# Optimization experiments

Measured on AMD Instinct MI355X. Metric: run time of the kernel, lower is better.

## Reference

```python
import jax, jax.numpy as jnp
import numpy as np

ALPHA = 1.0
GAMMA = 0.8
TAU = 0.1
NUM_SAMPLES = 10
TOP_K = 100
NUM_USER_GROUPS = 8
NUM_ITEM_GROUPS = 16
BATCH = 1024
NUM_ITEMS = 10000


def setup_inputs() -> dict:
    key = jax.random.key(0)
    k1, k2, k3, k4 = jax.random.split(key, 4)
    pred_scores = jax.random.normal(k1, (BATCH, NUM_ITEMS), dtype=jnp.float32)
    true_scores = jax.random.uniform(k2, (BATCH, NUM_ITEMS), dtype=jnp.float32)
    user_groups = jax.random.randint(k3, (BATCH,), 0, NUM_USER_GROUPS)
    item_groups = jax.random.randint(k4, (NUM_ITEMS,), 0, NUM_ITEM_GROUPS)
    return {
        "pred_scores": pred_scores,
        "true_scores": true_scores,
        "user_groups": user_groups,
        "item_groups": item_groups,
    }


def _calculate_exposure(scores):
    # scores: [B, k]. Soft-rank via Gumbel perturbations + pairwise sigmoid.
    B, k = scores.shape
    noise = jax.random.gumbel(jax.random.key(1), (NUM_SAMPLES, B, k), dtype=scores.dtype)
    noisy = scores[None, :, :] + noise                       # [S, B, k]
    diffs = noisy[..., :, None] - noisy[..., None, :]        # [S, B, k, k]
    # ranks = 1 + sum_j sigmoid((s_i - s_j)/tau) - sigmoid(0)
    ranks = 1.0 + jax.nn.sigmoid(diffs / TAU).sum(axis=-1) - 0.5  # [S, B, k]
    exposure = jnp.power(GAMMA, ranks - 1.0)                 # [S, B, k]
    return exposure.mean(axis=0)                             # [B, k]


def reference(pred_scores, true_scores, user_groups, item_groups):
    B = pred_scores.shape[0]
    # top-k selection (values == gathered pred scores)
    pred_topk, topk_idx = jax.lax.top_k(pred_scores, TOP_K)   # [B, k]
    item_groups_topk = item_groups[topk_idx]                  # [B, k]

    system_exposure = _calculate_exposure(pred_topk)          # [B, k]
    target_exposure = jnp.full_like(system_exposure, true_scores.mean())
    delta_E = system_exposure - target_exposure               # [B, k]

    ii_f_loss = jnp.mean(delta_E * delta_E)

    # group-pair scatter_mean
    pair_ids = user_groups[:, None] * NUM_ITEM_GROUPS + item_groups_topk  # [B, k]
    flat = delta_E.reshape(-1)
    pid = pair_ids.reshape(-1)
    num_pairs = NUM_USER_GROUPS * NUM_ITEM_GROUPS
    sums = jax.ops.segment_sum(flat, pid, num_segments=num_pairs)
    cnts = jax.ops.segment_sum(jnp.ones_like(flat), pid, num_segments=num_pairs)
    avg = jnp.where(cnts > 0, sums / jnp.maximum(cnts, 1.0), 0.0)
    gg_f_loss = jnp.mean(avg * avg)

    total_loss = ii_f_loss + ALPHA * gg_f_loss
    return (total_loss, ii_f_loss, gg_f_loss)
```

## Files before the change

kernel.cpp:

```cpp
#include <hip/hip_runtime.h>


typedef unsigned int u32;
typedef unsigned long long u64;

__device__ __forceinline__ u32 rotl32(u32 x, int r) { return (x << r) | (x >> (32 - r)); }

__device__ __forceinline__ void tf2x32(u32 k0, u32 k1, u32 x0, u32 x1, u32& o0, u32& o1) {
  u32 ks2 = 0x1BD11BDAu ^ k0 ^ k1;
#define TFR(r) { x0 += x1; x1 = rotl32(x1, r); x1 ^= x0; }
  x0 += k0; x1 += k1;
  TFR(13) TFR(15) TFR(26) TFR(6)
  x0 += k1; x1 += ks2 + 1u;
  TFR(17) TFR(29) TFR(16) TFR(24)
  x0 += ks2; x1 += k0 + 2u;
  TFR(13) TFR(15) TFR(26) TFR(6)
  x0 += k0; x1 += k1 + 3u;
  TFR(17) TFR(29) TFR(16) TFR(24)
  x0 += k1; x1 += ks2 + 4u;
  TFR(13) TFR(15) TFR(26) TFR(6)
  x0 += ks2; x1 += k0 + 5u;
#undef TFR
  o0 = x0; o1 = x1;
}

__device__ __forceinline__ float gumbel_noise(u32 i) {
  u32 o0, o1;
  tf2x32(0u, 1u, 0u, i, o0, o1);
  u32 bits = o0 ^ o1;
  float f = __uint_as_float((bits >> 9) | 0x3f800000u) - 1.0f;
  const float TINY = 1.17549435e-38f;
  float u = fmaxf(TINY, f + TINY);
  return -logf(-logf(u));
}

__device__ __forceinline__ u32 fkey(float v) {
  u32 u = __float_as_uint(v);
  return u ^ ((u & 0x80000000u) ? 0xFFFFFFFFu : 0x80000000u);
}

__global__ __launch_bounds__(256) void fused_kernel(
    const float* __restrict__ pred,
    const float* __restrict__ ts,
    const int*   __restrict__ ugrp,
    const int*   __restrict__ igrp,
    double* __restrict__ t_sum,
    double* __restrict__ sum_e, double* __restrict__ sum_e2,
    double* __restrict__ pair_sum, int* __restrict__ pair_cnt) {
  const int N = 10000, N4 = 2500, K = 100;
  const int b = blockIdx.x;
  const int t = threadIdx.x;

  __shared__ u32 hist[256];
  __shared__ u32 ckey[1024];
  __shared__ u64 sbuf[128];
  __shared__ float topv[100];
  __shared__ int   pidv[100];
  __shared__ __align__(16) float noisy[1000];
  __shared__ float expo[100];
  __shared__ float pairS[128];
  __shared__ int   pairC[128];
  __shared__ float wred[4];
  __shared__ u32 sh_cnt, sh_n2, sh_T, sh_A, sh_done;
  __shared__ float sh_bS, sh_bS2;

  hist[t] = 0u;
  if (t < 128) { pairS[t] = 0.f; pairC[t] = 0; }
  if (t < 100) expo[t] = 0.f;
  if (t == 0) { sh_cnt = 0u; sh_n2 = 0u; sh_done = 0u; sh_bS = 0.f; sh_bS2 = 0.f; }
  __syncthreads();

  const float4* row4 = (const float4*)(pred + (size_t)b * N);
  const float4* tsr4 = (const float4*)(ts + (size_t)b * N);

  float tsum = 0.f;
  for (int i4 = t; i4 < N4; i4 += 256) {
    float4 p = row4[i4];
    float4 q = tsr4[i4];
    tsum += (q.x + q.y) + (q.z + q.w);
    atomicAdd(&hist[fkey(p.x) >> 24], 1u);
    atomicAdd(&hist[fkey(p.y) >> 24], 1u);
    atomicAdd(&hist[fkey(p.z) >> 24], 1u);
    atomicAdd(&hist[fkey(p.w) >> 24], 1u);
  }
  for (int off = 32; off; off >>= 1) tsum += __shfl_down(tsum, off);
  if ((t & 63) == 0) wred[t >> 6] = tsum;
  __syncthreads();
  if (t == 0) {
    atomicAdd(t_sum, (double)((wred[0] + wred[1]) + (wred[2] + wred[3])));
    u32 cum = 0, b0 = 255;
    for (int v = 255; v >= 0; --v) {
      u32 c = hist[v];
      if (cum + c >= 100u) { b0 = (u32)v; break; }
      cum += c;
    }
    sh_A = cum;
    sh_T = b0 << 24;
    sh_done = (cum + hist[b0] <= 128u) ? 1u : 0u;
  }
  __syncthreads();

  if (!sh_done) {
    u32 b0 = sh_T >> 24;
    for (int i4 = t; i4 < N4; i4 += 256) {
      float4 p = row4[i4];
#pragma unroll
      for (int c = 0; c < 4; ++c) {
        float v = c == 0 ? p.x : c == 1 ? p.y : c == 2 ? p.z : p.w;
        u32 key = fkey(v);
        if ((key >> 24) == b0) {
          u32 pos = atomicAdd(&sh_cnt, 1u);
          if (pos < 1024u) ckey[pos] = key;
        }
      }
    }
    __syncthreads();
    u32 nk = sh_cnt < 1024u ? sh_cnt : 1024u;
    for (int shift = 16; shift >= 0; shift -= 8) {
      hist[t] = 0u;
      __syncthreads();
      u32 prefhi = sh_T >> (shift + 8);
      for (int i = t; i < (int)nk; i += 256) {
        u32 key = ckey[i];
        if ((key >> (shift + 8)) == prefhi) atomicAdd(&hist[(key >> shift) & 0xFFu], 1u);
      }
      __syncthreads();
      if (t == 0) {
        u32 target = 100u - sh_A;
        u32 cum = 0, bb = 255;
        for (int v = 255; v >= 0; --v) {
          u32 c = hist[v];
          if (cum + c >= target) { bb = (u32)v; break; }
          cum += c;
        }
        sh_A += cum;
        sh_T |= (u32)bb << shift;
        sh_done = (sh_A + hist[bb] <= 128u || shift == 0) ? 1u : 0u;
      }
      __syncthreads();
      if (sh_done) break;
    }
  }

  {
    u32 T = sh_T;
    for (int i4 = t; i4 < N4; i4 += 256) {
      float4 p = row4[i4];
#pragma unroll
      for (int c = 0; c < 4; ++c) {
        int i = i4 * 4 + c;
        float v = c == 0 ? p.x : c == 1 ? p.y : c == 2 ? p.z : p.w;
        u32 key = fkey(v);
        if (key >= T) {
          u32 pos = atomicAdd(&sh_n2, 1u);
          if (pos < 128u) sbuf[pos] = ((u64)key << 32) | (u32)(~(u32)i);
        }
      }
    }
    __syncthreads();
    u32 n2 = sh_n2 < 128u ? sh_n2 : 128u;
    if (t < 128 && (u32)t >= n2) sbuf[t] = 0ull;
    __syncthreads();
  }

  for (int k = 2; k <= 128; k <<= 1) {
    for (int j = k >> 1; j > 0; j >>= 1) {
      if (t < 128) {
        int ixj = t ^ j;
        if (ixj > t) {
          u64 a = sbuf[t], c2 = sbuf[ixj];
          bool up = (t & k) == 0;
          if (up ? (a < c2) : (a > c2)) { sbuf[t] = c2; sbuf[ixj] = a; }
        }
      }
      __syncthreads();
    }
  }

  int ug = ugrp[b];
  if (t < K) {
    u64 p = sbuf[t];
    u32 key = (u32)(p >> 32);
    u32 idx = ~(u32)p;
    u32 u = (key & 0x80000000u) ? (key ^ 0x80000000u) : ~key;
    topv[t] = __uint_as_float(u);
    pidv[t] = ug * 16 + igrp[idx];
  }
  __syncthreads();

  for (int si = t; si < 1000; si += 256) {
    int s = si / 100, i = si - s * 100;
    noisy[si] = topv[i] + gumbel_noise(((u32)s * 1024u + (u32)b) * 100u + (u32)i);
  }
  __syncthreads();

  const float C2 = 14.426950408889634f;
  const float LG = -0.32192809488736235f;
  for (int si = t; si < 1000; si += 256) {
    int s = si / 100, i = si - s * 100;
    float nv = noisy[si];
    float nvC = nv * C2;
    const float* nrow = &noisy[s * 100];
    float S = 0.f;
#pragma unroll 4
    for (int j = 0; j < 100; ++j) {
      float a = __builtin_fmaf(nrow[j], C2, -nvC);
      S += __builtin_amdgcn_rcpf(1.0f + exp2f(a));
    }
    float ex = exp2f((S - 0.5f) * LG);
    atomicAdd(&expo[i], ex);
  }
  __syncthreads();

  if (t < K) {
    float e = expo[t] * 0.1f;
    atomicAdd(&pairS[pidv[t]], e);
    atomicAdd(&pairC[pidv[t]], 1);
    atomicAdd(&sh_bS, e);
    atomicAdd(&sh_bS2, e * e);
  }
  __syncthreads();
  if (t < 128 && pairC[t] > 0) {
    atomicAdd(&pair_sum[t], (double)pairS[t]);
    atomicAdd(&pair_cnt[t], pairC[t]);
  }
  if (t == 0) {
    atomicAdd(sum_e, (double)sh_bS);
    atomicAdd(sum_e2, (double)sh_bS2);
  }
}

__global__ void finalize_kernel(const double* __restrict__ t_sum,
                                const double* __restrict__ sum_e,
                                const double* __restrict__ sum_e2,
                                const double* __restrict__ pair_sum,
                                const int* __restrict__ pair_cnt,
                                float* __restrict__ out) {
  if (threadIdx.x == 0 && blockIdx.x == 0) {
    double t = *t_sum / 10240000.0;
    double me = *sum_e / 102400.0;
    double me2 = *sum_e2 / 102400.0;
    double ii = me2 - 2.0 * t * me + t * t;
    double gg = 0.0;
    for (int p = 0; p < 128; ++p) {
      int c = pair_cnt[p];
      if (c > 0) {
        double avg = (pair_sum[p] - (double)c * t) / (double)c;
        gg += avg * avg;
      }
    }
    gg /= 128.0;
    out[0] = (float)(ii + gg);
    out[1] = (float)ii;
    out[2] = (float)gg;
  }
}

extern "C" void kernel_launch(void* const* d_in, const int* in_sizes, int n_in,
                              void* d_out, int out_size, void* d_ws, size_t ws_size,
                              hipStream_t stream) {
  (void)in_sizes; (void)n_in; (void)out_size; (void)ws_size;
  const float* pred = (const float*)d_in[0];
  const float* ts   = (const float*)d_in[1];
  const int*   ugrp = (const int*)d_in[2];
  const int*   igrp = (const int*)d_in[3];
  float* out = (float*)d_out;

  double* t_sum    = (double*)d_ws;
  double* sum_e    = t_sum + 1;
  double* sum_e2   = t_sum + 2;
  double* pair_sum = t_sum + 3;
  int*    pair_cnt = (int*)(t_sum + 3 + 128);

  hipMemsetAsync(d_ws, 0, (3 + 128) * sizeof(double) + 128 * sizeof(int), stream);

  fused_kernel<<<1024, 256, 0, stream>>>(pred, ts, ugrp, igrp,
                                         t_sum, sum_e, sum_e2, pair_sum, pair_cnt);
  finalize_kernel<<<1, 64, 0, stream>>>(t_sum, sum_e, sum_e2, pair_sum, pair_cnt, out);
}
```

Before: 208.0 us.

## Rework top-k radix select with wave-parallel bin search, candidate cache, rank sort

Raises the block size to 512 threads and splits the first histogram into four privatised copies to reduce LDS atomic contention. The serial single-thread bin scan is replaced by a 64-lane wave suffix-scan. Candidates at or above the first-level bin are cached with their indices, so later refinement and collection passes avoid re-reading global memory, with a global-memory fallback on overflow. The bitonic sort becomes a parallel rank-counting sort, the sigmoid inner loop uses float4 LDS reads, and the finalize kernel uses a parallel reduction. The larger block and extra shared arrays may cut occupancy.

```diff
diff --git a/kernel.cpp b/kernel.cpp
--- a/kernel.cpp
+++ b/kernel.cpp
@@ -39,7 +39,37 @@
   return u ^ ((u & 0x80000000u) ? 0xFFFFFFFFu : 0x80000000u);
 }
 
-__global__ __launch_bounds__(256) void fused_kernel(
+__device__ __forceinline__ void select_bin(const u32* __restrict__ hist, int shift,
+                                           u32* sh_T, u32* sh_A, u32* sh_done,
+                                           int lane) {
+  u32 prevA = *sh_A;
+  u32 target = 100u - prevA;
+  u32 c0 = hist[lane * 4 + 0], c1 = hist[lane * 4 + 1];
+  u32 c2 = hist[lane * 4 + 2], c3 = hist[lane * 4 + 3];
+  u32 s = c0 + c1 + c2 + c3;
+  u32 suf = s;
+#pragma unroll
+  for (int off = 1; off < 64; off <<= 1) {
+    u32 o = __shfl_down(suf, off);
+    suf += (lane + off < 64) ? o : 0u;
+  }
+  u32 sufx = suf - s;
+  if (sufx < target && suf >= target) {
+    u32 cc[4] = {c0, c1, c2, c3};
+    u32 acc = sufx, bin = 0, cnt = 0;
+#pragma unroll
+    for (int k = 3; k >= 0; --k) {
+      if (acc + cc[k] >= target) { bin = (u32)(lane * 4 + k); cnt = cc[k]; break; }
+      acc += cc[k];
+    }
+    u32 newA = prevA + acc;
+    *sh_T = *sh_T | (bin << shift);
+    *sh_A = newA;
+    *sh_done = (newA + cnt <= 128u || shift == 0) ? 1u : 0u;
+  }
+}
+
+__global__ __launch_bounds__(512, 8) void fused_kernel(
     const float* __restrict__ pred,
     const float* __restrict__ ts,
     const int*   __restrict__ ugrp,
@@ -51,92 +81,107 @@
   const int b = blockIdx.x;
   const int t = threadIdx.x;
 
-  __shared__ u32 hist[256];
-  __shared__ u32 ckey[1024];
+  __shared__ u32 hist4[4][256];
+  __shared__ u64 cand[2048];
   __shared__ u64 sbuf[128];
+  __shared__ u64 sorted[128];
+  __shared__ u32 rankv[128];
   __shared__ float topv[100];
   __shared__ int   pidv[100];
   __shared__ __align__(16) float noisy[1000];
   __shared__ float expo[100];
   __shared__ float pairS[128];
   __shared__ int   pairC[128];
-  __shared__ float wred[4];
-  __shared__ u32 sh_cnt, sh_n2, sh_T, sh_A, sh_done;
+  __shared__ float wred[8];
+  __shared__ u32 sh_cnt, sh_nc, sh_T, sh_A, sh_done, sh_ovf;
   __shared__ float sh_bS, sh_bS2;
 
-  hist[t] = 0u;
-  if (t < 128) { pairS[t] = 0.f; pairC[t] = 0; }
+  if (t < 256) { hist4[0][t] = 0u; hist4[1][t] = 0u; hist4[2][t] = 0u; hist4[3][t] = 0u; }
+  if (t < 128) { pairS[t] = 0.f; pairC[t] = 0; rankv[t] = 0u; }
   if (t < 100) expo[t] = 0.f;
-  if (t == 0) { sh_cnt = 0u; sh_n2 = 0u; sh_done = 0u; sh_bS = 0.f; sh_bS2 = 0.f; }
-  __syncthreads();
-
-  const float4* row4 = (const float4*)(pred + (size_t)b * N);
-  const float4* tsr4 = (const float4*)(ts + (size_t)b * N);
+  if (t == 0) { sh_cnt = 0u; sh_nc = 0u; sh_T = 0u; sh_A = 0u; sh_done = 0u; sh_ovf = 0u;
+                sh_bS = 0.f; sh_bS2 = 0.f; }
+  __syncthreads();
+
+  const float4* __restrict__ row4 = (const float4*)(pred + (size_t)b * N);
+  const float4* __restrict__ tsr4 = (const float4*)(ts + (size_t)b * N);
 
   float tsum = 0.f;
-  for (int i4 = t; i4 < N4; i4 += 256) {
-    float4 p = row4[i4];
-    float4 q = tsr4[i4];
-    tsum += (q.x + q.y) + (q.z + q.w);
-    atomicAdd(&hist[fkey(p.x) >> 24], 1u);
-    atomicAdd(&hist[fkey(p.y) >> 24], 1u);
-    atomicAdd(&hist[fkey(p.z) >> 24], 1u);
-    atomicAdd(&hist[fkey(p.w) >> 24], 1u);
-  }
+  u32* myh = hist4[(t >> 7) & 3];
+#pragma unroll
+  for (int k = 0; k < 5; ++k) {
+    int i4 = t + (k << 9);
+    if (k == 4 && i4 >= N4) break;
+    float4 pp = row4[i4];
+    float4 qq = tsr4[i4];
+    tsum += (qq.x + qq.y) + (qq.z + qq.w);
+    atomicAdd(&myh[fkey(pp.x) >> 24], 1u);
+    atomicAdd(&myh[fkey(pp.y) >> 24], 1u);
+    atomicAdd(&myh[fkey(pp.z) >> 24], 1u);
+    atomicAdd(&myh[fkey(pp.w) >> 24], 1u);
+  }
+#pragma unroll
   for (int off = 32; off; off >>= 1) tsum += __shfl_down(tsum, off);
   if ((t & 63) == 0) wred[t >> 6] = tsum;
   __syncthreads();
   if (t == 0) {
-    atomicAdd(t_sum, (double)((wred[0] + wred[1]) + (wred[2] + wred[3])));
-    u32 cum = 0, b0 = 255;
-    for (int v = 255; v >= 0; --v) {
-      u32 c = hist[v];
-      if (cum + c >= 100u) { b0 = (u32)v; break; }
-      cum += c;
-    }
-    sh_A = cum;
-    sh_T = b0 << 24;
-    sh_done = (cum + hist[b0] <= 128u) ? 1u : 0u;
-  }
-  __syncthreads();
-
-  if (!sh_done) {
+    float s8 = 0.f;
+#pragma unroll
+    for (int w = 0; w < 8; ++w) s8 += wred[w];
+    atomicAdd(t_sum, (double)s8);
+  }
+  if (t < 256) hist4[0][t] += hist4[1][t] + hist4[2][t] + hist4[3][t];
+  __syncthreads();
+
+  if (t < 64) select_bin(&hist4[0][0], 24, &sh_T, &sh_A, &sh_done, t);
+  __syncthreads();
+
+  bool r1done = (sh_done != 0u);
+  bool use_cand = false;
+  u32 nc = 0;
+
+  if (!r1done) {
     u32 b0 = sh_T >> 24;
-    for (int i4 = t; i4 < N4; i4 += 256) {
-      float4 p = row4[i4];
+    for (int i4 = t; i4 < N4; i4 += 512) {
+      float4 pp = row4[i4];
 #pragma unroll
       for (int c = 0; c < 4; ++c) {
-        float v = c == 0 ? p.x : c == 1 ? p.y : c == 2 ? p.z : p.w;
+        float v = (c == 0) ? pp.x : (c == 1) ? pp.y : (c == 2) ? pp.z : pp.w;
         u32 key = fkey(v);
-        if ((key >> 24) == b0) {
+        if ((key >> 24) >= b0) {
           u32 pos = atomicAdd(&sh_cnt, 1u);
-          if (pos < 1024u) ckey[pos] = key;
+          int idx = i4 * 4 + c;
+          if (pos < 2048u) cand[pos] = ((u64)key << 32) | (u32)(~(u32)idx);
+          else sh_ovf = 1u;
         }
       }
     }
     __syncthreads();
-    u32 nk = sh_cnt < 1024u ? sh_cnt : 1024u;
-    for (int shift = 16; shift >= 0; shift -= 8) {
-      hist[t] = 0u;
+    nc = sh_cnt < 2048u ? sh_cnt : 2048u;
+    use_cand = (sh_ovf == 0u);
+
+    for (int shift = 16; ; shift -= 8) {
+      if (t < 256) hist4[0][t] = 0u;
       __syncthreads();
-      u32 prefhi = sh_T >> (shift + 8);
-      for (int i = t; i < (int)nk; i += 256) {
-        u32 key = ckey[i];
-        if ((key >> (shift + 8)) == prefhi) atomicAdd(&hist[(key >> shift) & 0xFFu], 1u);
+      u32 pref = sh_T >> (shift + 8);
+      if (use_cand) {
+        for (int i = t; i < (int)nc; i += 512) {
+          u32 key = (u32)(cand[i] >> 32);
+          if ((key >> (shift + 8)) == pref) atomicAdd(&hist4[0][(key >> shift) & 255u], 1u);
+        }
+      } else {
+        for (int i4 = t; i4 < N4; i4 += 512) {
+          float4 pp = row4[i4];
+#pragma unroll
+          for (int c = 0; c < 4; ++c) {
+            float v = (c == 0) ? pp.x : (c == 1) ? pp.y : (c == 2) ? pp.z : pp.w;
+            u32 key = fkey(v);
+            if ((key >> (shift + 8)) == pref) atomicAdd(&hist4[0][(key >> shift) & 255u], 1u);
+          }
+        }
       }
       __syncthreads();
-      if (t == 0) {
-        u32 target = 100u - sh_A;
-        u32 cum = 0, bb = 255;
-        for (int v = 255; v >= 0; --v) {
-          u32 c = hist[v];
-          if (cum + c >= target) { bb = (u32)v; break; }
-          cum += c;
-        }
-        sh_A += cum;
-        sh_T |= (u32)bb << shift;
-        sh_done = (sh_A + hist[bb] <= 128u || shift == 0) ? 1u : 0u;
-      }
+      if (t < 64) select_bin(&hist4[0][0], shift, &sh_T, &sh_A, &sh_done, t);
       __syncthreads();
       if (sh_done) break;
     }
@@ -144,51 +189,60 @@
 
   {
     u32 T = sh_T;
-    for (int i4 = t; i4 < N4; i4 += 256) {
-      float4 p = row4[i4];
-#pragma unroll
-      for (int c = 0; c < 4; ++c) {
-        int i = i4 * 4 + c;
-        float v = c == 0 ? p.x : c == 1 ? p.y : c == 2 ? p.z : p.w;
-        u32 key = fkey(v);
-        if (key >= T) {
-          u32 pos = atomicAdd(&sh_n2, 1u);
-          if (pos < 128u) sbuf[pos] = ((u64)key << 32) | (u32)(~(u32)i);
+    if (use_cand) {
+      for (int i = t; i < (int)nc; i += 512) {
+        u64 p = cand[i];
+        if ((u32)(p >> 32) >= T) {
+          u32 pos = atomicAdd(&sh_nc, 1u);
+          if (pos < 128u) sbuf[pos] = p;
         }
       }
-    }
-    __syncthreads();
-    u32 n2 = sh_n2 < 128u ? sh_n2 : 128u;
-    if (t < 128 && (u32)t >= n2) sbuf[t] = 0ull;
-    __syncthreads();
-  }
-
-  for (int k = 2; k <= 128; k <<= 1) {
-    for (int j = k >> 1; j > 0; j >>= 1) {
-      if (t < 128) {
-        int ixj = t ^ j;
-        if (ixj > t) {
-          u64 a = sbuf[t], c2 = sbuf[ixj];
-          bool up = (t & k) == 0;
-          if (up ? (a < c2) : (a > c2)) { sbuf[t] = c2; sbuf[ixj] = a; }
+    } else {
+      for (int i4 = t; i4 < N4; i4 += 512) {
+        float4 pp = row4[i4];
+#pragma unroll
+        for (int c = 0; c < 4; ++c) {
+          float v = (c == 0) ? pp.x : (c == 1) ? pp.y : (c == 2) ? pp.z : pp.w;
+          u32 key = fkey(v);
+          if (key >= T) {
+            u32 pos = atomicAdd(&sh_nc, 1u);
+            int idx = i4 * 4 + c;
+            if (pos < 128u) sbuf[pos] = ((u64)key << 32) | (u32)(~(u32)idx);
+          }
         }
       }
-      __syncthreads();
-    }
+    }
+    __syncthreads();
+    u32 nreal = sh_nc < 128u ? sh_nc : 128u;
+    if (t < 128 && (u32)t >= nreal) sbuf[t] = 0ull;
+    __syncthreads();
+  }
+
+  {
+    int e = t >> 2, seg = t & 3;
+    u64 mykey = sbuf[e];
+    u32 cnt = 0;
+    int j0 = seg * 32;
+#pragma unroll 8
+    for (int j = j0; j < j0 + 32; ++j) cnt += (sbuf[j] > mykey) ? 1u : 0u;
+    if (cnt) atomicAdd(&rankv[e], cnt);
+    __syncthreads();
+    if (t < 128) sorted[rankv[t]] = sbuf[t];
+    __syncthreads();
   }
 
   int ug = ugrp[b];
   if (t < K) {
-    u64 p = sbuf[t];
-    u32 key = (u32)(p >> 32);
-    u32 idx = ~(u32)p;
+    u64 pk = sorted[t];
+    u32 key = (u32)(pk >> 32);
+    u32 idx = ~(u32)pk;
     u32 u = (key & 0x80000000u) ? (key ^ 0x80000000u) : ~key;
     topv[t] = __uint_as_float(u);
     pidv[t] = ug * 16 + igrp[idx];
   }
   __syncthreads();
 
-  for (int si = t; si < 1000; si += 256) {
+  for (int si = t; si < 1000; si += 512) {
     int s = si / 100, i = si - s * 100;
     noisy[si] = topv[i] + gumbel_noise(((u32)s * 1024u + (u32)b) * 100u + (u32)i);
   }
@@ -196,16 +250,18 @@
 
   const float C2 = 14.426950408889634f;
   const float LG = -0.32192809488736235f;
-  for (int si = t; si < 1000; si += 256) {
+  for (int si = t; si < 1000; si += 512) {
     int s = si / 100, i = si - s * 100;
-    float nv = noisy[si];
-    float nvC = nv * C2;
-    const float* nrow = &noisy[s * 100];
+    float nvC = noisy[si] * C2;
+    const float4* nr4 = (const float4*)(noisy + s * 100);
     float S = 0.f;
-#pragma unroll 4
-    for (int j = 0; j < 100; ++j) {
-      float a = __builtin_fmaf(nrow[j], C2, -nvC);
-      S += __builtin_amdgcn_rcpf(1.0f + exp2f(a));
+#pragma unroll 5
+    for (int jc = 0; jc < 25; ++jc) {
+      float4 nj = nr4[jc];
+      S += __builtin_amdgcn_rcpf(1.0f + exp2f(__builtin_fmaf(nj.x, C2, -nvC)));
+      S += __builtin_amdgcn_rcpf(1.0f + exp2f(__builtin_fmaf(nj.y, C2, -nvC)));
+      S += __builtin_amdgcn_rcpf(1.0f + exp2f(__builtin_fmaf(nj.z, C2, -nvC)));
+      S += __builtin_amdgcn_rcpf(1.0f + exp2f(__builtin_fmaf(nj.w, C2, -nvC)));
     }
     float ex = exp2f((S - 0.5f) * LG);
     atomicAdd(&expo[i], ex);
@@ -230,26 +286,31 @@
   }
 }
 
-__global__ void finalize_kernel(const double* __restrict__ t_sum,
-                                const double* __restrict__ sum_e,
-                                const double* __restrict__ sum_e2,
-                                const double* __restrict__ pair_sum,
-                                const int* __restrict__ pair_cnt,
-                                float* __restrict__ out) {
-  if (threadIdx.x == 0 && blockIdx.x == 0) {
-    double t = *t_sum / 10240000.0;
+__global__ __launch_bounds__(128) void finalize_kernel(
+    const double* __restrict__ t_sum, const double* __restrict__ sum_e,
+    const double* __restrict__ sum_e2, const double* __restrict__ pair_sum,
+    const int* __restrict__ pair_cnt, float* __restrict__ out) {
+  int t = threadIdx.x;
+  __shared__ double red[128];
+  double tmean = *t_sum / 10240000.0;
+  double g = 0.0;
+  int c = pair_cnt[t];
+  if (c > 0) {
+    double avg = (pair_sum[t] - (double)c * tmean) / (double)c;
+    g = avg * avg;
+  }
+  red[t] = g;
+  __syncthreads();
+#pragma unroll
+  for (int off = 64; off; off >>= 1) {
+    if (t < off) red[t] += red[t + off];
+    __syncthreads();
+  }
+  if (t == 0) {
+    double gg = red[0] / 128.0;
     double me = *sum_e / 102400.0;
     double me2 = *sum_e2 / 102400.0;
-    double ii = me2 - 2.0 * t * me + t * t;
-    double gg = 0.0;
-    for (int p = 0; p < 128; ++p) {
-      int c = pair_cnt[p];
-      if (c > 0) {
-        double avg = (pair_sum[p] - (double)c * t) / (double)c;
-        gg += avg * avg;
-      }
-    }
-    gg /= 128.0;
+    double ii = me2 - 2.0 * tmean * me + tmean * tmean;
     out[0] = (float)(ii + gg);
     out[1] = (float)ii;
     out[2] = (float)gg;
@@ -274,7 +335,7 @@
 
   hipMemsetAsync(d_ws, 0, (3 + 128) * sizeof(double) + 128 * sizeof(int), stream);
 
-  fused_kernel<<<1024, 256, 0, stream>>>(pred, ts, ugrp, igrp,
+  fused_kernel<<<1024, 512, 0, stream>>>(pred, ts, ugrp, igrp,
                                          t_sum, sum_e, sum_e2, pair_sum, pair_cnt);
-  finalize_kernel<<<1, 64, 0, stream>>>(t_sum, sum_e, sum_e2, pair_sum, pair_cnt, out);
-}
+  finalize_kernel<<<1, 128, 0, stream>>>(t_sum, sum_e, sum_e2, pair_sum, pair_cnt, out);
+}
```

Result: faster. 167.8 us (-19.3%).
